# Optimization experiments

Hardware: AMD Instinct MI355X
Metric: run time of the kernel (lower is better)

Reference implementation:

```python
import jax, jax.numpy as jnp
import numpy as np

B, L, D = 2, 2048, 1024
H = 16
HD = D // H  # 64


def _orthogonal_projection(key, d, m):
    g = jax.random.normal(key, (d, m), dtype=jnp.float32)
    q, r = jnp.linalg.qr(g)
    s = jnp.sign(jnp.diagonal(r))
    s = jnp.where(s == 0, 1.0, s)
    q = q * s[None, :]
    # preserve_variance=True
    return q * np.sqrt(d / m)


def setup_inputs() -> dict:
    key = jax.random.key(0)
    ks = jax.random.split(key, 8)
    x = jax.random.normal(ks[0], (B, L, D), dtype=jnp.float32)
    p = jax.random.normal(ks[1], (B, L, D), dtype=jnp.float32)
    s = 1.0 / np.sqrt(D)
    W_qkv = jax.random.uniform(ks[2], (3 * D, D), dtype=jnp.float32, minval=-s, maxval=s)
    b_qkv = jax.random.uniform(ks[3], (3 * D,), dtype=jnp.float32, minval=-s, maxval=s)
    W_out = jax.random.uniform(ks[4], (D, D), dtype=jnp.float32, minval=-s, maxval=s)
    b_out = jax.random.uniform(ks[5], (D,), dtype=jnp.float32, minval=-s, maxval=s)
    proj = _orthogonal_projection(ks[6], D, D // 2)
    return {"x": x, "p": p, "W_qkv": W_qkv, "b_qkv": b_qkv,
            "W_out": W_out, "b_out": b_out, "proj": proj}


def reference(x, p, W_qkv, b_qkv, W_out, b_out, proj):
    # QKV projection: (B,L,D) -> (B,L,3,H,HD)
    qkv = (jnp.einsum('bld,ed->ble', x, W_qkv) + b_qkv).reshape(B, L, 3, H, HD)
    q, k, v = qkv[:, :, 0], qkv[:, :, 1], qkv[:, :, 2]

    # Collaborative rotary phases from conditioning tokens: (B,L,H,HD/2)
    phases = (p @ proj).reshape(B, L, H, HD // 2)  # phase_scale = 1.0
    cos, sin = jnp.cos(phases), jnp.sin(phases)

    half = HD // 2
    # non-interleaved rotary: split head_dim into two halves
    def rot(t):
        t1, t2 = t[..., :half], t[..., half:]
        return jnp.concatenate([t1 * cos - t2 * sin, t1 * sin + t2 * cos], axis=-1)

    q, k = rot(q), rot(k)

    scale = HD ** -0.5
    scores = jnp.einsum('bqhd,bkhd->bhqk', q, k) * scale
    attn = jax.nn.softmax(scores, axis=-1)
    out = jnp.einsum('bhqk,bkhd->bqhd', attn, v).reshape(B, L, D)
    return jnp.einsum('bld,ed->ble', out, W_out) + b_out
```

## Files before the change

### kernel.cpp

```cpp
#include <hip/hip_runtime.h>
#include <hip/hip_bf16.h>
#include <math.h>

namespace {
constexpr int Bb = 2;
constexpr int Ll = 2048;
constexpr int Dd = 1024;
constexpr int Hh = 16;
constexpr int NT = Bb * Ll;
constexpr int D3 = 3 * Dd;
constexpr int PH = Dd / 2;
}

typedef __attribute__((ext_vector_type(8))) short bf16x8;
typedef __attribute__((ext_vector_type(4))) float f32x4;

__device__ inline unsigned pack2bf(float a, float b) {
  __hip_bfloat162 t = __float22bfloat162_rn(float2{a, b});
  union { __hip_bfloat162 h; unsigned u; } cv; cv.h = t;
  return cv.u;
}

__device__ inline float bfhalf(unsigned u, int hi) {
  union { unsigned u; float f; } c;
  c.u = hi ? (u & 0xffff0000u) : (u << 16);
  return c.f;
}

__device__ inline void async_cp16(const void* gsrc, void* ldst) {
  __builtin_amdgcn_global_load_lds(
      (const __attribute__((address_space(1))) unsigned int*)gsrc,
      (__attribute__((address_space(3))) unsigned int*)ldst, 16, 0, 0);
}

__global__ __launch_bounds__(256) void prep_kernel(
    const float4* __restrict__ p, uint2* __restrict__ p_hi4, uint2* __restrict__ p_lo4,
    const float* __restrict__ proj, short* __restrict__ th, short* __restrict__ tl,
    const float4* __restrict__ x, const float4* __restrict__ wq, const float4* __restrict__ wo,
    uint2* __restrict__ xd, uint2* __restrict__ wqd, uint2* __restrict__ wod)
{
  __shared__ float Ls[64][65];
  const int bid = blockIdx.x;
  const int tid = threadIdx.x;

  if (bid < 4096) {
    const int i = bid * 256 + tid;
    const float4 f = p[i];
    float hf[4], lf[4];
    const float ff[4] = {f.x, f.y, f.z, f.w};
#pragma unroll
    for (int j = 0; j < 4; ++j) {
      const __hip_bfloat16 h = __float2bfloat16(ff[j]);
      hf[j] = __bfloat162float(h);
      lf[j] = ff[j] - hf[j];
    }
    p_hi4[i] = make_uint2(pack2bf(hf[0], hf[1]), pack2bf(hf[2], hf[3]));
    p_lo4[i] = make_uint2(pack2bf(lf[0], lf[1]), pack2bf(lf[2], lf[3]));
  } else if (bid < 4224) {
    const int bx = bid - 4096;
    const int d0 = (bx & 15) * 64, m0 = (bx >> 4) * 64;
    const int r = tid >> 4, c4 = (tid & 15) * 4;
#pragma unroll
    for (int it = 0; it < 4; ++it) {
      const int row = it * 16 + r;
      const float4 v = *(const float4*)&proj[(size_t)(d0 + row) * PH + m0 + c4];
      Ls[row][c4] = v.x; Ls[row][c4+1] = v.y; Ls[row][c4+2] = v.z; Ls[row][c4+3] = v.w;
    }
    __syncthreads();
#pragma unroll
    for (int it = 0; it < 4; ++it) {
      const int row = it * 16 + r;
      float hf[4], lf[4];
#pragma unroll
      for (int j = 0; j < 4; ++j) {
        const float v = Ls[c4 + j][row];
        const __hip_bfloat16 h = __float2bfloat16(v);
        hf[j] = __bfloat162float(h);
        lf[j] = v - hf[j];
      }
      *(uint2*)&th[(size_t)(m0 + row) * Dd + d0 + c4] = make_uint2(pack2bf(hf[0], hf[1]), pack2bf(hf[2], hf[3]));
      *(uint2*)&tl[(size_t)(m0 + row) * Dd + d0 + c4] = make_uint2(pack2bf(lf[0], lf[1]), pack2bf(lf[2], lf[3]));
    }
  } else {
    int i = (bid - 4224) * 256 + tid;
    const float4* s; uint2* d;
    if (i < 1048576) { s = x; d = xd; }
    else if (i < 1048576 + 786432) { i -= 1048576; s = wq; d = wqd; }
    else { i -= 1048576 + 786432; s = wo; d = wod; }
    const float4 f = s[i];
    d[i] = make_uint2(pack2bf(f.x, f.y), pack2bf(f.z, f.w));
  }
}

__global__ __launch_bounds__(256) void gemm_nn_split(
    const short* __restrict__ Ah_g, const short* __restrict__ Al_g,
    const short* __restrict__ Wh_g, const short* __restrict__ Wl_g,
    float* __restrict__ C)
{
  __shared__ __align__(16) short Ah[3][64 * 32], Al[3][64 * 32];
  __shared__ __align__(16) short Wh[3][64 * 32], Wl[3][64 * 32];
  const int tid = threadIdx.x;
  const int w = tid >> 6, lane = tid & 63;
  const int l15 = lane & 15, quad = lane >> 4;
  const int n0 = blockIdx.y * 64, m0 = blockIdx.x * 64;

  const int row = tid >> 2, cc = tid & 3;
  const int ksw = (cc ^ (row & 3)) * 8;
  const short* gAh = Ah_g + (size_t)(n0 + row) * Dd + ksw;
  const short* gAl = Al_g + (size_t)(n0 + row) * Dd + ksw;
  const short* gWh = Wh_g + (size_t)(m0 + row) * Dd + ksw;
  const short* gWl = Wl_g + (size_t)(m0 + row) * Dd + ksw;

  f32x4 acc[4];
#pragma unroll
  for (int j = 0; j < 4; ++j) acc[j] = f32x4{0.f, 0.f, 0.f, 0.f};

  const int swq = (quad ^ (l15 & 3)) * 8;

#define STAGE_NN(kv, bf) { \
  async_cp16(gAh + (kv), &Ah[bf][tid * 8]); \
  async_cp16(gAl + (kv), &Al[bf][tid * 8]); \
  async_cp16(gWh + (kv), &Wh[bf][tid * 8]); \
  async_cp16(gWl + (kv), &Wl[bf][tid * 8]); }

  STAGE_NN(0, 0);
  STAGE_NN(32, 1);
  int bi = 0;
  for (int k0 = 0; k0 < Dd; k0 += 32) {
    if (k0 + 32 < Dd) { asm volatile("s_waitcnt vmcnt(4)" ::: "memory"); }
    else              { asm volatile("s_waitcnt vmcnt(0)" ::: "memory"); }
    __builtin_amdgcn_s_barrier();
    __builtin_amdgcn_sched_barrier(0);
    if (k0 + 64 < Dd) { const int bn = (bi + 2 >= 3) ? bi - 1 : bi + 2; STAGE_NN(k0 + 64, bn); }

    bf16x8 ah, al, wh[4], wl[4];
    ah = *(const bf16x8*)&Ah[bi][(w * 16 + l15) * 32 + swq];
    al = *(const bf16x8*)&Al[bi][(w * 16 + l15) * 32 + swq];
#pragma unroll
    for (int j = 0; j < 4; ++j) {
      wh[j] = *(const bf16x8*)&Wh[bi][(j * 16 + l15) * 32 + swq];
      wl[j] = *(const bf16x8*)&Wl[bi][(j * 16 + l15) * 32 + swq];
    }
#pragma unroll
    for (int j = 0; j < 4; ++j) {
      acc[j] = __builtin_amdgcn_mfma_f32_16x16x32_bf16(ah, wh[j], acc[j], 0, 0, 0);
      acc[j] = __builtin_amdgcn_mfma_f32_16x16x32_bf16(ah, wl[j], acc[j], 0, 0, 0);
      acc[j] = __builtin_amdgcn_mfma_f32_16x16x32_bf16(al, wh[j], acc[j], 0, 0, 0);
    }
    bi = (bi == 2) ? 0 : bi + 1;
  }
#undef STAGE_NN

#pragma unroll
  for (int r = 0; r < 4; ++r) {
    float* crow = C + (size_t)(n0 + w * 16 + quad * 4 + r) * PH + m0 + l15;
#pragma unroll
    for (int j = 0; j < 4; ++j) crow[j * 16] = acc[j][r];
  }
}

__global__ __launch_bounds__(256) void gemm_qkv_fused(
    const __hip_bfloat16* __restrict__ A, const __hip_bfloat16* __restrict__ W,
    const float* __restrict__ bias, const float* __restrict__ phases,
    __hip_bfloat16* __restrict__ q_bf, __hip_bfloat16* __restrict__ k_bf,
    __hip_bfloat16* __restrict__ vt_g)
{
  __shared__ __align__(16) short As[3][128 * 32];
  __shared__ __align__(16) short Ws[3][128 * 32];
  const int tid = threadIdx.x;
  const int w = tid >> 6, lane = tid & 63;
  const int l15 = lane & 15, quad = lane >> 4;
  const int wn = w >> 1, wm = w & 1;
  const int n0 = blockIdx.y * 128, m0 = blockIdx.x * 128;

  const int row = tid >> 2, cc = tid & 3;
  const int ksw = (cc ^ (row & 3)) * 8;
  const short* gA  = (const short*)A + (size_t)(n0 + row) * Dd + ksw;
  const short* gW  = (const short*)W + (size_t)(m0 + row) * Dd + ksw;

  f32x4 acc[4][4];
#pragma unroll
  for (int i = 0; i < 4; ++i)
#pragma unroll
    for (int j = 0; j < 4; ++j) acc[i][j] = f32x4{0.f, 0.f, 0.f, 0.f};

  const int swq = (quad ^ (l15 & 3)) * 8;

#define STAGE_QKV(kv, bf) { \
  async_cp16(gA + (kv),            &As[bf][tid * 8]); \
  async_cp16(gA + 64 * Dd + (kv),  &As[bf][2048 + tid * 8]); \
  async_cp16(gW + (kv),            &Ws[bf][tid * 8]); \
  async_cp16(gW + 64 * Dd + (kv),  &Ws[bf][2048 + tid * 8]); }

  STAGE_QKV(0, 0);
  STAGE_QKV(32, 1);
  int bi = 0;
  for (int k0 = 0; k0 < Dd; k0 += 32) {
    if (k0 + 32 < Dd) { asm volatile("s_waitcnt vmcnt(4)" ::: "memory"); }
    else              { asm volatile("s_waitcnt vmcnt(0)" ::: "memory"); }
    __builtin_amdgcn_s_barrier();
    __builtin_amdgcn_sched_barrier(0);
    if (k0 + 64 < Dd) { const int bn = (bi + 2 >= 3) ? bi - 1 : bi + 2; STAGE_QKV(k0 + 64, bn); }

    bf16x8 af[4], bf[4];
#pragma unroll
    for (int i = 0; i < 4; ++i)
      af[i] = *(const bf16x8*)&As[bi][(wn * 64 + i * 16 + l15) * 32 + swq];
#pragma unroll
    for (int j = 0; j < 4; ++j)
      bf[j] = *(const bf16x8*)&Ws[bi][(wm * 64 + j * 16 + l15) * 32 + swq];
#pragma unroll
    for (int i = 0; i < 4; ++i)
#pragma unroll
      for (int j = 0; j < 4; ++j)
        acc[i][j] = __builtin_amdgcn_mfma_f32_16x16x32_bf16(af[i], bf[j], acc[i][j], 0, 0, 0);
    bi = (bi == 2) ? 0 : bi + 1;
  }
#undef STAGE_QKV

  float bv[4];
#pragma unroll
  for (int j = 0; j < 4; ++j) bv[j] = bias[m0 + wm * 64 + j * 16 + l15];

  const int region = m0 >> 10;
  const int mloc = (m0 & 1023) + wm * 64;
  const int h = mloc >> 6;

  if (region < 2) {
    __hip_bfloat16* dst = region == 0 ? q_bf : k_bf;
    const float SC = region == 0 ? 0.18033688011112042f : 1.0f;
    const int dosw = (region == 1);
#pragma unroll
    for (int i = 0; i < 4; ++i)
#pragma unroll
      for (int r = 0; r < 4; ++r) {
        const int n = n0 + wn * 64 + i * 16 + quad * 4 + r;
        const int swz = dosw ? (((quad * 4 + r) & 7) << 3) : 0;
        const float* phrow = phases + (size_t)n * PH + h * 32;
        __hip_bfloat16* drow = dst + (size_t)n * Dd + h * 64;
#pragma unroll
        for (int pz = 0; pz < 2; ++pz) {
          const float ph = phrow[pz * 16 + l15];
          float sn, cs;
          __sincosf(ph, &sn, &cs);
          const float a1 = acc[i][pz][r] + bv[pz];
          const float a2 = acc[i][pz + 2][r] + bv[pz + 2];
          drow[(pz * 16 + l15) ^ swz]      = __float2bfloat16((a1 * cs - a2 * sn) * SC);
          drow[(pz * 16 + 32 + l15) ^ swz] = __float2bfloat16((a1 * sn + a2 * cs) * SC);
        }
      }
  } else {
    const int bh = (n0 >> 11) * 16 + h;
    const int tokb = (n0 & 2047) + wn * 64;
    const int vsw = (l15 & 7) << 3;
#pragma unroll
    for (int i = 0; i < 4; ++i)
#pragma unroll
      for (int j = 0; j < 4; ++j) {
        const uint2 o = make_uint2(
            pack2bf(acc[i][j][0] + bv[j], acc[i][j][1] + bv[j]),
            pack2bf(acc[i][j][2] + bv[j], acc[i][j][3] + bv[j]));
        const int d = j * 16 + l15;
        *(uint2*)&vt_g[(size_t)(bh * 64 + d) * Ll + tokb + ((i * 16 + quad * 4) ^ vsw)] = o;
      }
  }
}

__global__ __launch_bounds__(256) void gemm_bt_64(
    const __hip_bfloat16* __restrict__ A, const __hip_bfloat16* __restrict__ W,
    const float* __restrict__ bias, float* __restrict__ C, int K, int M)
{
  __shared__ __align__(16) short As[3][128 * 32];
  __shared__ __align__(16) short Ws[3][64 * 32];
  const int tid = threadIdx.x;
  const int w = tid >> 6, lane = tid & 63;
  const int l15 = lane & 15, quad = lane >> 4;
  const int n0 = blockIdx.y * 128, m0 = blockIdx.x * 64;

  const int row = tid >> 2, cc = tid & 3;
  const int ksw = (cc ^ (row & 3)) * 8;
  const short* gA = (const short*)A + (size_t)(n0 + row) * K + ksw;
  const short* gW = (const short*)W + (size_t)(m0 + row) * K + ksw;

  f32x4 acc[2][4];
#pragma unroll
  for (int i = 0; i < 2; ++i)
#pragma unroll
    for (int j = 0; j < 4; ++j) acc[i][j] = f32x4{0.f, 0.f, 0.f, 0.f};

  const int swq = (quad ^ (l15 & 3)) * 8;

#define STAGE_BT(kv, bf) { \
  async_cp16(gA + (kv),           &As[bf][tid * 8]); \
  async_cp16(gA + 64 * K + (kv),  &As[bf][2048 + tid * 8]); \
  async_cp16(gW + (kv),           &Ws[bf][tid * 8]); }

  STAGE_BT(0, 0);
  STAGE_BT(32, 1);
  int bi = 0;
  for (int k0 = 0; k0 < K; k0 += 32) {
    if (k0 + 32 < K) { asm volatile("s_waitcnt vmcnt(3)" ::: "memory"); }
    else             { asm volatile("s_waitcnt vmcnt(0)" ::: "memory"); }
    __builtin_amdgcn_s_barrier();
    __builtin_amdgcn_sched_barrier(0);
    if (k0 + 64 < K) { const int bn = (bi + 2 >= 3) ? bi - 1 : bi + 2; STAGE_BT(k0 + 64, bn); }

    bf16x8 af[2], bf[4];
#pragma unroll
    for (int i = 0; i < 2; ++i)
      af[i] = *(const bf16x8*)&As[bi][(w * 32 + i * 16 + l15) * 32 + swq];
#pragma unroll
    for (int j = 0; j < 4; ++j)
      bf[j] = *(const bf16x8*)&Ws[bi][(j * 16 + l15) * 32 + swq];
#pragma unroll
    for (int i = 0; i < 2; ++i)
#pragma unroll
      for (int j = 0; j < 4; ++j)
        acc[i][j] = __builtin_amdgcn_mfma_f32_16x16x32_bf16(af[i], bf[j], acc[i][j], 0, 0, 0);
    bi = (bi == 2) ? 0 : bi + 1;
  }
#undef STAGE_BT

  float bv[4];
#pragma unroll
  for (int j = 0; j < 4; ++j) bv[j] = bias[m0 + j * 16 + l15];
#pragma unroll
  for (int i = 0; i < 2; ++i)
#pragma unroll
    for (int r = 0; r < 4; ++r) {
      float* crow = C + (size_t)(n0 + w * 32 + i * 16 + quad * 4 + r) * M + m0 + l15;
#pragma unroll
      for (int j = 0; j < 4; ++j) crow[j * 16] = acc[i][j][r] + bv[j];
    }
}

__global__ __launch_bounds__(256) void attn_mfma(
    const __hip_bfloat16* __restrict__ q_bf,
    const __hip_bfloat16* __restrict__ k_bf,
    const __hip_bfloat16* __restrict__ vt_g,
    __hip_bfloat16* __restrict__ o_part,
    float* __restrict__ lden_g)
{
  __shared__ __align__(16) short Kb[2][4096];
  __shared__ __align__(16) short Vb[2][4096];

  const int tid = threadIdx.x;
  const int w = tid >> 6;
  const int lane = tid & 63;
  const int l15 = lane & 15;
  const int quad = lane >> 4;

  const int q0 = blockIdx.x * 128;
  const int bh = blockIdx.y;
  const int kz = blockIdx.z;
  const int b = bh >> 4, h = bh & 15;
  const int kt0 = kz * 16;

  bf16x8 qfrag[2][2];
#pragma unroll
  for (int qg = 0; qg < 2; ++qg)
#pragma unroll
    for (int kh = 0; kh < 2; ++kh) {
      const size_t qrow = (size_t)(b * Ll + q0 + w * 32 + qg * 16 + l15);
      qfrag[qg][kh] = *(const bf16x8*)(q_bf + qrow * Dd + h * 64 + kh * 32 + quad * 8);
    }

  f32x4 acc[4][2];
#pragma unroll
  for (int dt = 0; dt < 4; ++dt)
#pragma unroll
    for (int qg = 0; qg < 2; ++qg) acc[dt][qg] = f32x4{0.f, 0.f, 0.f, 0.f};
  f32x4 lden[2] = {f32x4{0.f,0.f,0.f,0.f}, f32x4{0.f,0.f,0.f,0.f}};
  const f32x4 zro = {0.f, 0.f, 0.f, 0.f};
  const short one_bf = (short)0x3F80;
  const bf16x8 ones8 = {one_bf, one_bf, one_bf, one_bf, one_bf, one_bf, one_bf, one_bf};

  const __hip_bfloat16* ksrc = k_bf + ((size_t)(b * Ll) + (tid >> 3)) * Dd + h * 64 + (tid & 7) * 8;
  const __hip_bfloat16* vsrc = vt_g + ((size_t)(bh * 64) + (tid >> 3)) * Ll + (tid & 7) * 8;
  const int ldst = tid * 8;

  const int sw = (l15 & 7) << 3;
  const int co0 = (quad * 8) ^ sw;
  const int co1 = (32 + quad * 8) ^ sw;

#define STAGE_K(t, bf) { const __hip_bfloat16* kp_ = ksrc + (size_t)(t) * 64 * Dd; \
  async_cp16(kp_, &Kb[bf][ldst]); async_cp16(kp_ + (size_t)32 * Dd, &Kb[bf][2048 + ldst]); }
#define STAGE_V(t, bf) { const __hip_bfloat16* vp_ = vsrc + (size_t)(t) * 64; \
  async_cp16(vp_, &Vb[bf][ldst]); async_cp16(vp_ + (size_t)32 * Ll, &Vb[bf][2048 + ldst]); }

  f32x4 s[4][2];

#define QK_N(Ks, n) { \
  const bf16x8 af0_ = *(const bf16x8*)&(Ks)[((n) * 16 + l15) * 64 + co0]; \
  const bf16x8 af1_ = *(const bf16x8*)&(Ks)[((n) * 16 + l15) * 64 + co1]; \
  s[n][0] = __builtin_amdgcn_mfma_f32_16x16x32_bf16(af0_, qfrag[0][0], zro, 0, 0, 0); \
  s[n][1] = __builtin_amdgcn_mfma_f32_16x16x32_bf16(af0_, qfrag[1][0], zro, 0, 0, 0); \
  s[n][0] = __builtin_amdgcn_mfma_f32_16x16x32_bf16(af1_, qfrag[0][1], s[n][0], 0, 0, 0); \
  s[n][1] = __builtin_amdgcn_mfma_f32_16x16x32_bf16(af1_, qfrag[1][1], s[n][1], 0, 0, 0); }

#define EXPPACK(v, dst) { union { float f; unsigned u; } p0_, p1_, p2_, p3_; \
  p0_.f = __builtin_amdgcn_exp2f((v)[0]); p1_.f = __builtin_amdgcn_exp2f((v)[1]); \
  p2_.f = __builtin_amdgcn_exp2f((v)[2]); p3_.f = __builtin_amdgcn_exp2f((v)[3]); \
  dst = make_uint2(__builtin_amdgcn_perm(p1_.u, p0_.u, 0x07060302u), \
                   __builtin_amdgcn_perm(p3_.u, p2_.u, 0x07060302u)); }

#define PV_QG(va, aU, cU, qg) { \
  auto rx32_ = __builtin_amdgcn_permlane32_swap((aU).x, (cU).x, false, false); \
  auto rx16_ = __builtin_amdgcn_permlane16_swap(rx32_[0], rx32_[1], false, false); \
  auto ry32_ = __builtin_amdgcn_permlane32_swap((aU).y, (cU).y, false, false); \
  auto ry16_ = __builtin_amdgcn_permlane16_swap(ry32_[0], ry32_[1], false, false); \
  union { unsigned u[4]; bf16x8 v; } pb_; \
  pb_.u[0] = rx16_[0]; pb_.u[1] = ry16_[0]; pb_.u[2] = rx16_[1]; pb_.u[3] = ry16_[1]; \
  lden[qg] = __builtin_amdgcn_mfma_f32_16x16x32_bf16(ones8, pb_.v, lden[qg], 0, 0, 0); \
  acc[0][qg] = __builtin_amdgcn_mfma_f32_16x16x32_bf16(va[0], pb_.v, acc[0][qg], 0, 0, 0); \
  acc[1][qg] = __builtin_amdgcn_mfma_f32_16x16x32_bf16(va[1], pb_.v, acc[1][qg], 0, 0, 0); \
  acc[2][qg] = __builtin_amdgcn_mfma_f32_16x16x32_bf16(va[2], pb_.v, acc[2][qg], 0, 0, 0); \
  acc[3][qg] = __builtin_amdgcn_mfma_f32_16x16x32_bf16(va[3], pb_.v, acc[3][qg], 0, 0, 0); }

  STAGE_K(kt0, 0);
  __syncthreads();
  STAGE_K(kt0 + 1, 1);
  STAGE_V(kt0, 0);
  __builtin_amdgcn_s_setprio(1);
  QK_N(Kb[0], 0); QK_N(Kb[0], 1); QK_N(Kb[0], 2); QK_N(Kb[0], 3);
  __builtin_amdgcn_s_setprio(0);

  for (int i = 0; i < 16; ++i) {
    __syncthreads();
    if (i + 2 < 16) STAGE_K(kt0 + i + 2, i & 1);
    if (i + 1 < 16) STAGE_V(kt0 + i + 1, (i + 1) & 1);
    const short* Kn = &Kb[(i + 1) & 1][0];
    const short* Vc = &Vb[i & 1][0];
    const bool doqk = (i + 1 < 16);

    uint2 a0, a1, c0, c1;
    EXPPACK(s[0][0], a0); EXPPACK(s[0][1], a1);
    EXPPACK(s[1][0], c0); EXPPACK(s[1][1], c1);
    if (doqk) {
      __builtin_amdgcn_s_setprio(1);
      QK_N(Kn, 0); QK_N(Kn, 1);
      __builtin_amdgcn_s_setprio(0);
    }
    {
      bf16x8 va[4];
#pragma unroll
      for (int dt = 0; dt < 4; ++dt)
        va[dt] = *(const bf16x8*)&Vc[(dt * 16 + l15) * 64 + co0];
      __builtin_amdgcn_s_setprio(1);
      PV_QG(va, a0, c0, 0);
      PV_QG(va, a1, c1, 1);
      __builtin_amdgcn_s_setprio(0);
    }

    uint2 a2, a3, c2, c3;
    EXPPACK(s[2][0], a2); EXPPACK(s[2][1], a3);
    EXPPACK(s[3][0], c2); EXPPACK(s[3][1], c3);
    if (doqk) {
      __builtin_amdgcn_s_setprio(1);
      QK_N(Kn, 2); QK_N(Kn, 3);
      __builtin_amdgcn_s_setprio(0);
    }
    {
      bf16x8 va[4];
#pragma unroll
      for (int dt = 0; dt < 4; ++dt)
        va[dt] = *(const bf16x8*)&Vc[(dt * 16 + l15) * 64 + co1];
      __builtin_amdgcn_s_setprio(1);
      PV_QG(va, a2, c2, 0);
      PV_QG(va, a3, c3, 1);
      __builtin_amdgcn_s_setprio(0);
    }
  }

#undef STAGE_K
#undef STAGE_V
#undef QK_N
#undef EXPPACK
#undef PV_QG

#pragma unroll
  for (int qg = 0; qg < 2; ++qg) {
    const float lv = lden[qg][0];
    const float linv = 1.f / lv;
    const int ql = q0 + w * 32 + qg * 16 + l15;
    if (quad == 0)
      lden_g[((size_t)(kz * Bb + b) * Hh + h) * Ll + ql] = lv;
    __hip_bfloat16* dst = o_part + ((size_t)kz * NT + b * Ll + ql) * Dd + h * 64;
#pragma unroll
    for (int dt = 0; dt < 4; ++dt) {
      const uint2 o = make_uint2(
          pack2bf(acc[dt][qg][0] * linv, acc[dt][qg][1] * linv),
          pack2bf(acc[dt][qg][2] * linv, acc[dt][qg][3] * linv));
      *(uint2*)&dst[dt * 16 + quad * 4] = o;
    }
  }
}

__global__ __launch_bounds__(256) void attn_combine(
    const __hip_bfloat16* __restrict__ o_part, const float* __restrict__ lden_g,
    __hip_bfloat16* __restrict__ aout)
{
  const int i = blockIdx.x * 256 + threadIdx.x;
  const int n = i >> 8, d4 = i & 255;
  const int b = n >> 11, l = n & 2047;
  const int h = d4 >> 4;
  const float l0 = lden_g[((size_t)b * Hh + h) * Ll + l];
  const float l1 = lden_g[((size_t)(Bb + b) * Hh + h) * Ll + l];
  const float inv = 1.f / (l0 + l1);
  const float w0 = l0 * inv, w1 = l1 * inv;
  const uint2 a0 = ((const uint2*)o_part)[i];
  const uint2 a1 = ((const uint2*)o_part)[(NT * (size_t)Dd / 4) + i];
  const float r0 = w0 * bfhalf(a0.x, 0) + w1 * bfhalf(a1.x, 0);
  const float r1 = w0 * bfhalf(a0.x, 1) + w1 * bfhalf(a1.x, 1);
  const float r2 = w0 * bfhalf(a0.y, 0) + w1 * bfhalf(a1.y, 0);
  const float r3 = w0 * bfhalf(a0.y, 1) + w1 * bfhalf(a1.y, 1);
  ((uint2*)aout)[i] = make_uint2(pack2bf(r0, r1), pack2bf(r2, r3));
}

extern "C" void kernel_launch(void* const* d_in, const int* in_sizes, int n_in,
                              void* d_out, int out_size, void* d_ws, size_t ws_size,
                              hipStream_t stream) {
  const float* x     = (const float*)d_in[0];
  const float* p     = (const float*)d_in[1];
  const float* W_qkv = (const float*)d_in[2];
  const float* b_qkv = (const float*)d_in[3];
  const float* W_out = (const float*)d_in[4];
  const float* b_out = (const float*)d_in[5];
  const float* proj  = (const float*)d_in[6];
  float* out = (float*)d_out;

  char* wsb = (char*)d_ws;
  float*          phases   = (float*)(wsb);
  short*          p_hi     = (short*)(wsb + (8u << 20));
  __hip_bfloat16* aout_bf  = (__hip_bfloat16*)(wsb + (8u << 20));
  short*          p_lo     = (short*)(wsb + (16u << 20));
  __hip_bfloat16* vt_g     = (__hip_bfloat16*)(wsb + (16u << 20));
  short*          projt_hi = (short*)(wsb + (24u << 20));
  short*          projt_lo = (short*)(wsb + (25u << 20));
  __hip_bfloat16* q_bf     = (__hip_bfloat16*)(wsb + (26u << 20));
  __hip_bfloat16* k_bf     = (__hip_bfloat16*)(wsb + (34u << 20));
  __hip_bfloat16* x_bf     = (__hip_bfloat16*)(wsb + (42u << 20));
  __hip_bfloat16* o_part   = (__hip_bfloat16*)(wsb + (42u << 20));
  __hip_bfloat16* wqkv_bf  = (__hip_bfloat16*)(wsb + (50u << 20));
  __hip_bfloat16* wout_bf  = (__hip_bfloat16*)(wsb + (58u << 20));
  float*          lden_g   = (float*)(wsb + (60u << 20));

  prep_kernel<<<12416, 256, 0, stream>>>(
      (const float4*)p, (uint2*)p_hi, (uint2*)p_lo,
      proj, projt_hi, projt_lo,
      (const float4*)x, (const float4*)W_qkv, (const float4*)W_out,
      (uint2*)x_bf, (uint2*)wqkv_bf, (uint2*)wout_bf);
  gemm_nn_split<<<dim3(PH / 64, NT / 64), 256, 0, stream>>>(p_hi, p_lo, projt_hi, projt_lo, phases);
  gemm_qkv_fused<<<dim3(D3 / 128, NT / 128), 256, 0, stream>>>(x_bf, wqkv_bf, b_qkv, phases,
                                                               q_bf, k_bf, vt_g);
  attn_mfma<<<dim3(Ll / 128, Bb * Hh, 2), 256, 0, stream>>>(q_bf, k_bf, vt_g, o_part, lden_g);
  attn_combine<<<4096, 256, 0, stream>>>(o_part, lden_g, aout_bf);
  gemm_bt_64<<<dim3(Dd / 64, NT / 128), 256, 0, stream>>>(aout_bf, wout_bf, b_out, out, Dd, Dd);
}
```

Baseline: 252.8 us.

## Fuse split-K attention combine into output projection GEMM A-tile loading

Removes the separate attn_combine kernel. The output GEMM now reads both split-K partial outputs and their softmax denominators, merges them in registers, and writes the combined bf16 A tile to LDS with a register-prefetched double buffer, while W still streams through async LDS loads. This drops one launch and the round trip of the combined activation through global memory. In exchange the GEMM reads twice the A data, and because there are 16 column blocks, the merge is redone once per column block. Sched barriers are also removed from the two other GEMM loops.

```diff
diff --git a/kernel.cpp b/kernel.cpp
--- a/kernel.cpp
+++ b/kernel.cpp
@@ -25,6 +25,12 @@
   union { unsigned u; float f; } c;
   c.u = hi ? (u & 0xffff0000u) : (u << 16);
   return c.f;
+}
+
+__device__ inline unsigned merge2(unsigned u0, unsigned u1, float w0, float w1) {
+  const float r0 = w0 * bfhalf(u0, 0) + w1 * bfhalf(u1, 0);
+  const float r1 = w0 * bfhalf(u0, 1) + w1 * bfhalf(u1, 1);
+  return pack2bf(r0, r1);
 }
 
 __device__ inline void async_cp16(const void* gsrc, void* ldst) {
@@ -130,7 +136,6 @@
     if (k0 + 32 < Dd) { asm volatile("s_waitcnt vmcnt(4)" ::: "memory"); }
     else              { asm volatile("s_waitcnt vmcnt(0)" ::: "memory"); }
     __builtin_amdgcn_s_barrier();
-    __builtin_amdgcn_sched_barrier(0);
     if (k0 + 64 < Dd) { const int bn = (bi + 2 >= 3) ? bi - 1 : bi + 2; STAGE_NN(k0 + 64, bn); }
 
     bf16x8 ah, al, wh[4], wl[4];
@@ -199,7 +204,6 @@
     if (k0 + 32 < Dd) { asm volatile("s_waitcnt vmcnt(4)" ::: "memory"); }
     else              { asm volatile("s_waitcnt vmcnt(0)" ::: "memory"); }
     __builtin_amdgcn_s_barrier();
-    __builtin_amdgcn_sched_barrier(0);
     if (k0 + 64 < Dd) { const int bn = (bi + 2 >= 3) ? bi - 1 : bi + 2; STAGE_QKV(k0 + 64, bn); }
 
     bf16x8 af[4], bf[4];
@@ -266,11 +270,13 @@
   }
 }
 
-__global__ __launch_bounds__(256) void gemm_bt_64(
-    const __hip_bfloat16* __restrict__ A, const __hip_bfloat16* __restrict__ W,
-    const float* __restrict__ bias, float* __restrict__ C, int K, int M)
+__global__ __launch_bounds__(256) void gemm_bt_fused(
+    const __hip_bfloat16* __restrict__ o_part,
+    const float* __restrict__ lden_g,
+    const __hip_bfloat16* __restrict__ W,
+    const float* __restrict__ bias, float* __restrict__ C)
 {
-  __shared__ __align__(16) short As[3][128 * 32];
+  __shared__ __align__(16) short As[2][128 * 32];
   __shared__ __align__(16) short Ws[3][64 * 32];
   const int tid = threadIdx.x;
   const int w = tid >> 6, lane = tid & 63;
@@ -279,8 +285,18 @@
 
   const int row = tid >> 2, cc = tid & 3;
   const int ksw = (cc ^ (row & 3)) * 8;
-  const short* gA = (const short*)A + (size_t)(n0 + row) * K + ksw;
-  const short* gW = (const short*)W + (size_t)(m0 + row) * K + ksw;
+  const short* gW = (const short*)W + (size_t)(m0 + row) * Dd + ksw;
+
+  const int nA = n0 + row, nB = n0 + 64 + row;
+  const __hip_bfloat16* gA = o_part + (size_t)nA * Dd + ksw;
+  const __hip_bfloat16* gB = o_part + (size_t)nB * Dd + ksw;
+  constexpr size_t ZOFF = (size_t)NT * Dd;
+  const int bA = nA >> 11, lAi = nA & 2047;
+  const int bB = nB >> 11, lBi = nB & 2047;
+  const float* ldA0 = lden_g + (size_t)bA * Hh * Ll + lAi;
+  const float* ldA1 = lden_g + (size_t)(Bb + bA) * Hh * Ll + lAi;
+  const float* ldB0 = lden_g + (size_t)bB * Hh * Ll + lBi;
+  const float* ldB1 = lden_g + (size_t)(Bb + bB) * Hh * Ll + lBi;
 
   f32x4 acc[2][4];
 #pragma unroll
@@ -290,36 +306,62 @@
 
   const int swq = (quad ^ (l15 & 3)) * 8;
 
-#define STAGE_BT(kv, bf) { \
-  async_cp16(gA + (kv),           &As[bf][tid * 8]); \
-  async_cp16(gA + 64 * K + (kv),  &As[bf][2048 + tid * 8]); \
-  async_cp16(gW + (kv),           &Ws[bf][tid * 8]); }
-
-  STAGE_BT(0, 0);
-  STAGE_BT(32, 1);
-  int bi = 0;
-  for (int k0 = 0; k0 < K; k0 += 32) {
-    if (k0 + 32 < K) { asm volatile("s_waitcnt vmcnt(3)" ::: "memory"); }
-    else             { asm volatile("s_waitcnt vmcnt(0)" ::: "memory"); }
-    __builtin_amdgcn_s_barrier();
-    __builtin_amdgcn_sched_barrier(0);
-    if (k0 + 64 < K) { const int bn = (bi + 2 >= 3) ? bi - 1 : bi + 2; STAGE_BT(k0 + 64, bn); }
+  uint4 pa0, pa1, pb0, pb1;
+  float wl0, wl1, wl2, wl3;
+
+#define ISSUE_W(kv, bf) async_cp16(gW + (kv), &Ws[bf][tid * 8]);
+#define LD_LDEN(kv) { const int h_ = ((kv) + ksw) >> 6; \
+  wl0 = ldA0[(size_t)h_ * Ll]; wl1 = ldA1[(size_t)h_ * Ll]; \
+  wl2 = ldB0[(size_t)h_ * Ll]; wl3 = ldB1[(size_t)h_ * Ll]; }
+#define LD_A(kv) { pa0 = *(const uint4*)(gA + (kv)); pa1 = *(const uint4*)(gA + ZOFF + (kv)); \
+  pb0 = *(const uint4*)(gB + (kv)); pb1 = *(const uint4*)(gB + ZOFF + (kv)); }
+#define MERGE_WRITE(buf) { \
+  const float iA_ = 1.f / (wl0 + wl1); const float w0A_ = wl0 * iA_, w1A_ = wl1 * iA_; \
+  const float iB_ = 1.f / (wl2 + wl3); const float w0B_ = wl2 * iB_, w1B_ = wl3 * iB_; \
+  uint4 mA_, mB_; \
+  mA_.x = merge2(pa0.x, pa1.x, w0A_, w1A_); mA_.y = merge2(pa0.y, pa1.y, w0A_, w1A_); \
+  mA_.z = merge2(pa0.z, pa1.z, w0A_, w1A_); mA_.w = merge2(pa0.w, pa1.w, w0A_, w1A_); \
+  mB_.x = merge2(pb0.x, pb1.x, w0B_, w1B_); mB_.y = merge2(pb0.y, pb1.y, w0B_, w1B_); \
+  mB_.z = merge2(pb0.z, pb1.z, w0B_, w1B_); mB_.w = merge2(pb0.w, pb1.w, w0B_, w1B_); \
+  *(uint4*)&As[buf][tid * 8] = mA_; *(uint4*)&As[buf][2048 + tid * 8] = mB_; }
+
+  ISSUE_W(0, 0);
+  LD_LDEN(0); LD_A(0);
+  MERGE_WRITE(0);
+  ISSUE_W(32, 1);
+  LD_LDEN(32); LD_A(32);
+  asm volatile("s_waitcnt lgkmcnt(0)" ::: "memory");
+  __builtin_amdgcn_s_barrier();
+
+  for (int i = 0; i < 32; ++i) {
+    const int k0 = i * 32;
+    const int cur = i & 1;
+    if (i + 2 < 32) ISSUE_W(k0 + 64, (i + 2) % 3);
 
     bf16x8 af[2], bf[4];
 #pragma unroll
-    for (int i = 0; i < 2; ++i)
-      af[i] = *(const bf16x8*)&As[bi][(w * 32 + i * 16 + l15) * 32 + swq];
+    for (int ii = 0; ii < 2; ++ii)
+      af[ii] = *(const bf16x8*)&As[cur][(w * 32 + ii * 16 + l15) * 32 + swq];
 #pragma unroll
     for (int j = 0; j < 4; ++j)
-      bf[j] = *(const bf16x8*)&Ws[bi][(j * 16 + l15) * 32 + swq];
-#pragma unroll
-    for (int i = 0; i < 2; ++i)
+      bf[j] = *(const bf16x8*)&Ws[i % 3][(j * 16 + l15) * 32 + swq];
+#pragma unroll
+    for (int ii = 0; ii < 2; ++ii)
 #pragma unroll
       for (int j = 0; j < 4; ++j)
-        acc[i][j] = __builtin_amdgcn_mfma_f32_16x16x32_bf16(af[i], bf[j], acc[i][j], 0, 0, 0);
-    bi = (bi == 2) ? 0 : bi + 1;
-  }
-#undef STAGE_BT
+        acc[ii][j] = __builtin_amdgcn_mfma_f32_16x16x32_bf16(af[ii], bf[j], acc[ii][j], 0, 0, 0);
+
+    if (i + 1 < 32) MERGE_WRITE(cur ^ 1);
+    if (i + 2 < 32) { LD_LDEN(k0 + 64); LD_A(k0 + 64); }
+    if (i + 1 < 32) {
+      asm volatile("s_waitcnt lgkmcnt(0)" ::: "memory");
+      __builtin_amdgcn_s_barrier();
+    }
+  }
+#undef ISSUE_W
+#undef LD_LDEN
+#undef LD_A
+#undef MERGE_WRITE
 
   float bv[4];
 #pragma unroll
@@ -328,7 +370,7 @@
   for (int i = 0; i < 2; ++i)
 #pragma unroll
     for (int r = 0; r < 4; ++r) {
-      float* crow = C + (size_t)(n0 + w * 32 + i * 16 + quad * 4 + r) * M + m0 + l15;
+      float* crow = C + (size_t)(n0 + w * 32 + i * 16 + quad * 4 + r) * Dd + m0 + l15;
 #pragma unroll
       for (int j = 0; j < 4; ++j) crow[j * 16] = acc[i][j][r] + bv[j];
     }
@@ -496,27 +538,6 @@
   }
 }
 
-__global__ __launch_bounds__(256) void attn_combine(
-    const __hip_bfloat16* __restrict__ o_part, const float* __restrict__ lden_g,
-    __hip_bfloat16* __restrict__ aout)
-{
-  const int i = blockIdx.x * 256 + threadIdx.x;
-  const int n = i >> 8, d4 = i & 255;
-  const int b = n >> 11, l = n & 2047;
-  const int h = d4 >> 4;
-  const float l0 = lden_g[((size_t)b * Hh + h) * Ll + l];
-  const float l1 = lden_g[((size_t)(Bb + b) * Hh + h) * Ll + l];
-  const float inv = 1.f / (l0 + l1);
-  const float w0 = l0 * inv, w1 = l1 * inv;
-  const uint2 a0 = ((const uint2*)o_part)[i];
-  const uint2 a1 = ((const uint2*)o_part)[(NT * (size_t)Dd / 4) + i];
-  const float r0 = w0 * bfhalf(a0.x, 0) + w1 * bfhalf(a1.x, 0);
-  const float r1 = w0 * bfhalf(a0.x, 1) + w1 * bfhalf(a1.x, 1);
-  const float r2 = w0 * bfhalf(a0.y, 0) + w1 * bfhalf(a1.y, 0);
-  const float r3 = w0 * bfhalf(a0.y, 1) + w1 * bfhalf(a1.y, 1);
-  ((uint2*)aout)[i] = make_uint2(pack2bf(r0, r1), pack2bf(r2, r3));
-}
-
 extern "C" void kernel_launch(void* const* d_in, const int* in_sizes, int n_in,
                               void* d_out, int out_size, void* d_ws, size_t ws_size,
                               hipStream_t stream) {
@@ -532,7 +553,6 @@
   char* wsb = (char*)d_ws;
   float*          phases   = (float*)(wsb);
   short*          p_hi     = (short*)(wsb + (8u << 20));
-  __hip_bfloat16* aout_bf  = (__hip_bfloat16*)(wsb + (8u << 20));
   short*          p_lo     = (short*)(wsb + (16u << 20));
   __hip_bfloat16* vt_g     = (__hip_bfloat16*)(wsb + (16u << 20));
   short*          projt_hi = (short*)(wsb + (24u << 20));
@@ -554,6 +574,5 @@
   gemm_qkv_fused<<<dim3(D3 / 128, NT / 128), 256, 0, stream>>>(x_bf, wqkv_bf, b_qkv, phases,
                                                                q_bf, k_bf, vt_g);
   attn_mfma<<<dim3(Ll / 128, Bb * Hh, 2), 256, 0, stream>>>(q_bf, k_bf, vt_g, o_part, lden_g);
-  attn_combine<<<4096, 256, 0, stream>>>(o_part, lden_g, aout_bf);
-  gemm_bt_64<<<dim3(Dd / 64, NT / 128), 256, 0, stream>>>(aout_bf, wout_bf, b_out, out, Dd, Dd);
-}
+  gemm_bt_fused<<<dim3(Dd / 64, NT / 128), 256, 0, stream>>>(o_part, lden_g, wout_bf, b_out, out);
+}
```

Measured after the change: 260.5 us. +3.0%, slower.
